# Kernel optimization log

Hardware: AMD Instinct MI355X
Metric: run time of the kernel (lower is better)

Reference implementation:

```python
import jax, jax.numpy as jnp
import numpy as np
import math

EPS = 1e-6
NUM_HEADS = 8


def _layernorm(x, g, b):
    mu = jnp.mean(x, axis=-1, keepdims=True)
    var = jnp.mean(jnp.square(x - mu), axis=-1, keepdims=True)
    return (x - mu) * jax.lax.rsqrt(var + EPS) * g + b


def _pos_embed(n, d):
    pos = jnp.arange(n, dtype=jnp.float32)[:, None]                  # [N,1]
    div = jnp.exp(jnp.arange(0, d, 2, dtype=jnp.float32) * (-math.log(10000.0) / d))
    ang = pos * div                                                  # [N,d/2]
    pe = jnp.stack([jnp.sin(ang), jnp.cos(ang)], axis=-1).reshape(n, d)
    return pe


def setup_inputs() -> dict:
    key = jax.random.key(0)
    B, N, C, L = 2, 2048, 256, 4
    ks = jax.random.split(key, 6)
    s = 0.02
    return {
        "x": jax.random.normal(ks[0], (B, N, C), jnp.float32),
        "qkv_w": jax.random.normal(ks[1], (L, C, 3 * C), jnp.float32) * s,
        "proj_w": jax.random.normal(ks[2], (L, C, C), jnp.float32) * s,
        "proj_b": jnp.zeros((L, C), jnp.float32),
        "w1": jax.random.normal(ks[3], (L, C, C), jnp.float32) * s,
        "b1": jnp.zeros((L, C), jnp.float32),
        "w2": jax.random.normal(ks[4], (L, C, C), jnp.float32) * s,
        "b2": jnp.zeros((L, C), jnp.float32),
        "g1": jnp.ones((L, C), jnp.float32),
        "be1": jnp.zeros((L, C), jnp.float32),
        "g2": jnp.ones((L, C), jnp.float32),
        "be2": jnp.zeros((L, C), jnp.float32),
    }


def reference(x, qkv_w, proj_w, proj_b, w1, b1, w2, b2, g1, be1, g2, be2):
    B, N, C = x.shape
    L = qkv_w.shape[0]
    H = NUM_HEADS
    dh = C // H
    scale = dh ** -0.5

    x = x + _pos_embed(N, C)[None]

    for l in range(L):
        # --- attention (manual QKV, post-norm residual as in source) ---
        qkv = (x @ qkv_w[l]).reshape(B, N, 3, H, dh)
        q, k, v = qkv[:, :, 0], qkv[:, :, 1], qkv[:, :, 2]           # [B,N,H,dh]
        attn = jnp.einsum('bqhd,bkhd->bhqk', q, k) * scale           # [B,H,N,N]
        attn = jax.nn.softmax(attn, axis=-1)
        o = jnp.einsum('bhqk,bkhd->bqhd', attn, v).reshape(B, N, C)
        o = o @ proj_w[l] + proj_b[l]
        x = _layernorm(x + o, g1[l], be1[l])
        # --- MLP (GELU exact, as torch nn.GELU default) ---
        m = jax.nn.gelu(x @ w1[l] + b1[l], approximate=False) @ w2[l] + b2[l]
        x = _layernorm(x + m, g2[l], be2[l])
    return x
```

## Files before the change

### kernel.cpp

```cpp
#include <hip/hip_runtime.h>
#include <math.h>

#define Bd 2
#define Nd 2048
#define Cd 256
#define Ld 4
#define Hd 8
#define Md (Bd*Nd)
#define BHd 16
#define U32d 1024
#define SPLITd 4

typedef __attribute__((ext_vector_type(8))) short bf16x8;
typedef __attribute__((ext_vector_type(4))) float f32x4;
typedef __attribute__((ext_vector_type(16))) float f32x16;
typedef __attribute__((ext_vector_type(4))) short shortx4;

static __device__ inline f32x4 mfma16(bf16x8 a, bf16x8 b, f32x4 c) {
    return __builtin_amdgcn_mfma_f32_16x16x32_bf16(a, b, c, 0, 0, 0);
}
static __device__ inline f32x16 mfma32(bf16x8 a, bf16x8 b, f32x16 c) {
    return __builtin_amdgcn_mfma_f32_32x32x16_bf16(a, b, c, 0, 0, 0);
}
static __device__ inline short f2bf(float f) {
    union { float f; unsigned u; } v; v.f = f;
    unsigned r = (v.u + 0x7fff + ((v.u >> 16) & 1)) >> 16;
    return (short)r;
}
static __device__ inline unsigned pkbf(float a, float b) {
    unsigned r;
    asm("v_cvt_pk_bf16_f32 %0, %1, %2" : "=v"(r) : "v"(a), "v"(b));
    return r;
}

__global__ __launch_bounds__(256)
void wtrans_kernel(const float* __restrict__ src, short* __restrict__ dst,
                   int Nc, float scale, int scaleLim)
{
    __shared__ float tile[32][33];
    int l = blockIdx.z;
    src += (size_t)l * 256 * Nc;
    dst += (size_t)l * Nc * 256;
    int c0 = blockIdx.x * 32, k0 = blockIdx.y * 32;
    int tx = threadIdx.x & 31, ty = threadIdx.x >> 5;
#pragma unroll
    for (int i = 0; i < 4; i++) {
        int k = ty + 8 * i;
        tile[k][tx] = src[(size_t)(k0 + k) * Nc + c0 + tx];
    }
    __syncthreads();
#pragma unroll
    for (int i = 0; i < 4; i++) {
        int cc = ty + 8 * i;
        int col = c0 + cc;
        float v = tile[tx][cc];
        if (col < scaleLim) v *= scale;
        dst[(size_t)col * 256 + k0 + tx] = f2bf(v);
    }
}

__global__ __launch_bounds__(256)
void pos_add_kernel(const float* __restrict__ xin, float* __restrict__ xf,
                    short* __restrict__ xb)
{
    int i = blockIdx.x * 256 + threadIdx.x;
    int c = i & (Cd - 1);
    int n = (i >> 8) & (Nd - 1);
    const float kneg = -9.210340371976184f / 256.0f;
    float div = __expf((float)(c & ~1) * kneg);
    float ang = (float)n * div;
    float pe = (c & 1) ? cosf(ang) : sinf(ang);
    float v = xin[i] + pe;
    xf[i] = v;
    xb[i] = f2bf(v);
}

__global__ __launch_bounds__(256)
void qkv_gemm_kernel(const short* __restrict__ Ab, const short* __restrict__ WT,
                     short* __restrict__ Qb, short* __restrict__ Kb,
                     short* __restrict__ Vtb)
{
    int t = threadIdx.x, w = t >> 6, l = t & 63, c = l & 15, g = l >> 4;
    int rowBase = blockIdx.y * 128 + w * 32;
    int colBase = blockIdx.x * 32;
    const f32x4 zero = {0.f, 0.f, 0.f, 0.f};
    f32x4 acc[2][2] = {{zero, zero}, {zero, zero}};
    const short* ap0 = Ab + (size_t)(rowBase + c) * 256 + g * 8;
    const short* ap1 = ap0 + 16 * 256;
    const short* bp0 = WT + (size_t)(colBase + c) * 256 + g * 8;
    const short* bp1 = bp0 + 16 * 256;
#pragma unroll
    for (int kc = 0; kc < 256; kc += 32) {
        bf16x8 a0 = *(const bf16x8*)(ap0 + kc);
        bf16x8 a1 = *(const bf16x8*)(ap1 + kc);
        bf16x8 b0 = *(const bf16x8*)(bp0 + kc);
        bf16x8 b1 = *(const bf16x8*)(bp1 + kc);
        acc[0][0] = mfma16(a0, b0, acc[0][0]);
        acc[0][1] = mfma16(a0, b1, acc[0][1]);
        acc[1][0] = mfma16(a1, b0, acc[1][0]);
        acc[1][1] = mfma16(a1, b1, acc[1][1]);
    }
    int region = colBase >> 8;
    if (region < 2) {
        short* dst = (region == 0) ? Qb : Kb;
        int cb = colBase - region * 256;
#pragma unroll
        for (int m = 0; m < 2; m++)
#pragma unroll
            for (int n = 0; n < 2; n++)
#pragma unroll
                for (int r = 0; r < 4; r++)
                    dst[(size_t)(rowBase + 16 * m + 4 * g + r) * 256 + cb + 16 * n + c]
                        = f2bf(acc[m][n][r]);
    } else {
        int b = rowBase >> 11;
        int ntok0 = (rowBase & (Nd - 1)) + 4 * g;
#pragma unroll
        for (int m = 0; m < 2; m++)
#pragma unroll
            for (int n = 0; n < 2; n++) {
                int chg = colBase - 512 + 16 * n + c;
                shortx4 pkv;
#pragma unroll
                for (int r = 0; r < 4; r++) pkv[r] = f2bf(acc[m][n][r]);
                *(shortx4*)&Vtb[(size_t)((b * Hd + (chg >> 5)) * 32 + (chg & 31)) * Nd
                                + ntok0 + 16 * m] = pkv;
            }
    }
}

__global__ __launch_bounds__(256)
void attn_part_kernel(const short* __restrict__ Qb, const short* __restrict__ Kb,
                      const short* __restrict__ Vtb, float* __restrict__ OP,
                      float* __restrict__ Lsum)
{
    int t = threadIdx.x, w = t >> 6, l = t & 63;
    int l5 = l >> 5, q32 = l & 31;
    bool low = (l5 == 0);
    int qt = blockIdx.x * 4 + w;
    int bh = blockIdx.y, part = blockIdx.z;
    int b = bh >> 3, h = bh & 7;

    bf16x8 qf0, qf1;
    {
        const short* qp = Qb + ((size_t)(b * Nd + qt * 32 + q32)) * 256 + h * 32 + 8 * l5;
        qf0 = *(const bf16x8*)qp;
        qf1 = *(const bf16x8*)(qp + 16);
    }
    const short* kp = Kb + (size_t)b * Nd * 256 + h * 32 + 8 * l5;
    const short* vp = Vtb + (size_t)(bh * 32 + q32) * Nd + 8 * l5;

    f32x16 O;
#pragma unroll
    for (int i = 0; i < 16; i++) O[i] = 0.f;
    float lsum = 0.f;

    const int kstart = part * (Nd / SPLITd);
    const int kend = (part + 1) * (Nd / SPLITd);

    bf16x8 kf[2][2], vv[4];
#pragma unroll
    for (int sb = 0; sb < 2; sb++)
#pragma unroll
        for (int ks = 0; ks < 2; ks++)
            kf[sb][ks] = *(const bf16x8*)(kp + (size_t)(kstart + 32 * sb + q32) * 256 + 16 * ks);
#pragma unroll
    for (int kc = 0; kc < 4; kc++)
        vv[kc] = *(const bf16x8*)(vp + kstart + 16 * kc);

    for (int k0 = kstart; k0 < kend; k0 += 64) {
        int kn = (k0 + 64 < kend) ? (k0 + 64) : k0;
        bf16x8 kfn[2][2], vvn[4];
#pragma unroll
        for (int sb = 0; sb < 2; sb++)
#pragma unroll
            for (int ks = 0; ks < 2; ks++)
                kfn[sb][ks] = *(const bf16x8*)(kp + (size_t)(kn + 32 * sb + q32) * 256 + 16 * ks);
#pragma unroll
        for (int kc = 0; kc < 4; kc++)
            vvn[kc] = *(const bf16x8*)(vp + kn + 16 * kc);

#pragma unroll
        for (int sb = 0; sb < 2; sb++) {
            f32x16 s;
#pragma unroll
            for (int i = 0; i < 16; i++) s[i] = 0.f;
            s = mfma32(kf[sb][0], qf0, s);
            s = mfma32(kf[sb][1], qf1, s);
            float ps = 0.f;
#pragma unroll
            for (int i = 0; i < 16; i++) { s[i] = exp2f(s[i]); ps += s[i]; }
            ps += __shfl_xor(ps, 32, 64);
            lsum += ps;
            unsigned wd[8];
#pragma unroll
            for (int i = 0; i < 8; i++) wd[i] = pkbf(s[2 * i], s[2 * i + 1]);
#pragma unroll
            for (int half = 0; half < 2; half++) {
                int b0 = 4 * half;
                unsigned sx0 = (unsigned)__shfl_xor((int)wd[b0], 32, 64);
                unsigned sx1 = (unsigned)__shfl_xor((int)wd[b0 + 1], 32, 64);
                unsigned sx2 = (unsigned)__shfl_xor((int)wd[b0 + 2], 32, 64);
                unsigned sx3 = (unsigned)__shfl_xor((int)wd[b0 + 3], 32, 64);
                union { unsigned u[4]; bf16x8 v; } pa;
                pa.u[0] = low ? wd[b0] : sx2;
                pa.u[1] = low ? wd[b0 + 1] : sx3;
                pa.u[2] = low ? sx0 : wd[b0 + 2];
                pa.u[3] = low ? sx1 : wd[b0 + 3];
                O = mfma32(pa.v, vv[2 * sb + half], O);
            }
        }
#pragma unroll
        for (int sb = 0; sb < 2; sb++)
#pragma unroll
            for (int ks = 0; ks < 2; ks++) kf[sb][ks] = kfn[sb][ks];
#pragma unroll
        for (int kc = 0; kc < 4; kc++) vv[kc] = vvn[kc];
    }

    int u = bh * 64 + qt;
    float* op = OP + ((size_t)part * U32d + u) * 1024;
#pragma unroll
    for (int i = 0; i < 16; i++) {
        int q = (i & 3) + 8 * (i >> 2) + 4 * l5;
        op[q * 32 + q32] = O[i];
    }
    if (low) Lsum[((size_t)part * U32d + u) * 32 + q32] = lsum;
}

__global__ __launch_bounds__(512)
void proj_ln_kernel(const float* __restrict__ OP, const float* __restrict__ Lsum,
                    const short* __restrict__ WT, const float* __restrict__ bias,
                    const float* __restrict__ resid, const float* __restrict__ gg,
                    const float* __restrict__ be, float* __restrict__ outf,
                    short* __restrict__ outb)
{
    __shared__ short Atile[16 * 264];
    __shared__ float red[8][16][2];
    int t = threadIdx.x;
    int rowBase = blockIdx.x * 16;

    {
        int r = t >> 5, seg = t & 31;
        int grow = rowBase + r;
        int bb = grow >> 11;
        int qt = (grow & (Nd - 1)) >> 5;
        int q = grow & 31;
        int h = seg >> 2;
        int dh0 = (seg & 3) * 8;
        int u = (bb * Hd + h) * 64 + qt;
        float o[8] = {0.f, 0.f, 0.f, 0.f, 0.f, 0.f, 0.f, 0.f};
        float L = 0.f;
#pragma unroll
        for (int p = 0; p < SPLITd; p++) {
            const float* src = OP + ((size_t)p * U32d + u) * 1024 + q * 32 + dh0;
            float4 v0 = *(const float4*)src;
            float4 v1 = *(const float4*)(src + 4);
            o[0] += v0.x; o[1] += v0.y; o[2] += v0.z; o[3] += v0.w;
            o[4] += v1.x; o[5] += v1.y; o[6] += v1.z; o[7] += v1.w;
            L += Lsum[((size_t)p * U32d + u) * 32 + q];
        }
        float inv = 1.f / L;
        bf16x8 pk;
#pragma unroll
        for (int j = 0; j < 8; j++) pk[j] = f2bf(o[j] * inv);
        *(bf16x8*)&Atile[r * 264 + seg * 8] = pk;
    }
    __syncthreads();

    int w = t >> 6, l = t & 63, c = l & 15, g = l >> 4;
    const f32x4 zero = {0.f, 0.f, 0.f, 0.f};
    f32x4 acc0 = zero, acc1 = zero;
    const short* bp0 = WT + (size_t)(w * 32 + c) * 256 + g * 8;
    const short* bp1 = bp0 + 16 * 256;
#pragma unroll
    for (int kc = 0; kc < 256; kc += 32) {
        bf16x8 a = *(const bf16x8*)&Atile[c * 264 + g * 8 + kc];
        acc0 = mfma16(a, *(const bf16x8*)(bp0 + kc), acc0);
        acc1 = mfma16(a, *(const bf16x8*)(bp1 + kc), acc1);
    }

    float vv[2][4], s_[4] = {0.f, 0.f, 0.f, 0.f}, sq_[4] = {0.f, 0.f, 0.f, 0.f};
    int col0 = w * 32 + c, col1 = col0 + 16;
    float bi0 = bias[col0], bi1 = bias[col1];
#pragma unroll
    for (int r = 0; r < 4; r++) {
        int row = rowBase + 4 * g + r;
        float v0 = acc0[r] + bi0 + resid[(size_t)row * 256 + col0];
        float v1 = acc1[r] + bi1 + resid[(size_t)row * 256 + col1];
        vv[0][r] = v0; vv[1][r] = v1;
        s_[r] += v0 + v1; sq_[r] += v0 * v0 + v1 * v1;
    }
#pragma unroll
    for (int off = 1; off <= 8; off <<= 1)
#pragma unroll
        for (int r = 0; r < 4; r++) {
            s_[r] += __shfl_xor(s_[r], off, 64);
            sq_[r] += __shfl_xor(sq_[r], off, 64);
        }
    if (c == 0)
#pragma unroll
        for (int r = 0; r < 4; r++) {
            red[w][4 * g + r][0] = s_[r];
            red[w][4 * g + r][1] = sq_[r];
        }
    __syncthreads();
    float mu[4], rs[4];
#pragma unroll
    for (int r = 0; r < 4; r++) {
        float S = 0.f, Q = 0.f;
#pragma unroll
        for (int ww = 0; ww < 8; ww++) { S += red[ww][4 * g + r][0]; Q += red[ww][4 * g + r][1]; }
        mu[r] = S * (1.f / 256.f);
        rs[r] = rsqrtf(Q * (1.f / 256.f) - mu[r] * mu[r] + 1e-6f);
    }
    float gv0 = gg[col0], bv0 = be[col0], gv1 = gg[col1], bv1 = be[col1];
#pragma unroll
    for (int r = 0; r < 4; r++) {
        int row = rowBase + 4 * g + r;
        float o0 = (vv[0][r] - mu[r]) * rs[r] * gv0 + bv0;
        float o1 = (vv[1][r] - mu[r]) * rs[r] * gv1 + bv1;
        outf[(size_t)row * 256 + col0] = o0;
        outf[(size_t)row * 256 + col1] = o1;
        outb[(size_t)row * 256 + col0] = f2bf(o0);
        outb[(size_t)row * 256 + col1] = f2bf(o1);
    }
}

template<int LAST>
__global__ __launch_bounds__(512)
void mlp_kernel(const short* __restrict__ xbin, const short* __restrict__ W1T,
                const float* __restrict__ b1, const short* __restrict__ W2T,
                const float* __restrict__ b2, const float* __restrict__ resid,
                const float* __restrict__ gg, const float* __restrict__ be,
                float* __restrict__ outf, short* __restrict__ outb)
{
    __shared__ short A1[16 * 264];
    __shared__ short A2[16 * 264];
    __shared__ float red[8][16][2];
    int t = threadIdx.x;
    int rowBase = blockIdx.x * 16;

    {
        int r = t >> 5, seg = t & 31;
        *(bf16x8*)&A1[r * 264 + seg * 8] =
            *(const bf16x8*)(xbin + (size_t)(rowBase + r) * 256 + seg * 8);
    }
    __syncthreads();

    int w = t >> 6, l = t & 63, c = l & 15, g = l >> 4;
    const f32x4 zero = {0.f, 0.f, 0.f, 0.f};
    int col0 = w * 32 + c, col1 = col0 + 16;

    {
        f32x4 acc0 = zero, acc1 = zero;
        const short* bp0 = W1T + (size_t)(w * 32 + c) * 256 + g * 8;
        const short* bp1 = bp0 + 16 * 256;
#pragma unroll
        for (int kc = 0; kc < 256; kc += 32) {
            bf16x8 a = *(const bf16x8*)&A1[c * 264 + g * 8 + kc];
            acc0 = mfma16(a, *(const bf16x8*)(bp0 + kc), acc0);
            acc1 = mfma16(a, *(const bf16x8*)(bp1 + kc), acc1);
        }
        float bi0 = b1[col0], bi1 = b1[col1];
#pragma unroll
        for (int r = 0; r < 4; r++) {
            float v0 = acc0[r] + bi0, v1 = acc1[r] + bi1;
            v0 = 0.5f * v0 * (1.f + erff(v0 * 0.7071067811865476f));
            v1 = 0.5f * v1 * (1.f + erff(v1 * 0.7071067811865476f));
            A2[(4 * g + r) * 264 + col0] = f2bf(v0);
            A2[(4 * g + r) * 264 + col1] = f2bf(v1);
        }
    }
    __syncthreads();

    f32x4 acc0 = zero, acc1 = zero;
    const short* bp0 = W2T + (size_t)(w * 32 + c) * 256 + g * 8;
    const short* bp1 = bp0 + 16 * 256;
#pragma unroll
    for (int kc = 0; kc < 256; kc += 32) {
        bf16x8 a = *(const bf16x8*)&A2[c * 264 + g * 8 + kc];
        acc0 = mfma16(a, *(const bf16x8*)(bp0 + kc), acc0);
        acc1 = mfma16(a, *(const bf16x8*)(bp1 + kc), acc1);
    }
    float vv[2][4], s_[4] = {0.f, 0.f, 0.f, 0.f}, sq_[4] = {0.f, 0.f, 0.f, 0.f};
    float bi0 = b2[col0], bi1 = b2[col1];
#pragma unroll
    for (int r = 0; r < 4; r++) {
        int row = rowBase + 4 * g + r;
        float v0 = acc0[r] + bi0 + resid[(size_t)row * 256 + col0];
        float v1 = acc1[r] + bi1 + resid[(size_t)row * 256 + col1];
        vv[0][r] = v0; vv[1][r] = v1;
        s_[r] += v0 + v1; sq_[r] += v0 * v0 + v1 * v1;
    }
#pragma unroll
    for (int off = 1; off <= 8; off <<= 1)
#pragma unroll
        for (int r = 0; r < 4; r++) {
            s_[r] += __shfl_xor(s_[r], off, 64);
            sq_[r] += __shfl_xor(sq_[r], off, 64);
        }
    if (c == 0)
#pragma unroll
        for (int r = 0; r < 4; r++) {
            red[w][4 * g + r][0] = s_[r];
            red[w][4 * g + r][1] = sq_[r];
        }
    __syncthreads();
    float mu[4], rs[4];
#pragma unroll
    for (int r = 0; r < 4; r++) {
        float S = 0.f, Q = 0.f;
#pragma unroll
        for (int ww = 0; ww < 8; ww++) { S += red[ww][4 * g + r][0]; Q += red[ww][4 * g + r][1]; }
        mu[r] = S * (1.f / 256.f);
        rs[r] = rsqrtf(Q * (1.f / 256.f) - mu[r] * mu[r] + 1e-6f);
    }
    float gv0 = gg[col0], bv0 = be[col0], gv1 = gg[col1], bv1 = be[col1];
#pragma unroll
    for (int r = 0; r < 4; r++) {
        int row = rowBase + 4 * g + r;
        float o0 = (vv[0][r] - mu[r]) * rs[r] * gv0 + bv0;
        float o1 = (vv[1][r] - mu[r]) * rs[r] * gv1 + bv1;
        outf[(size_t)row * 256 + col0] = o0;
        outf[(size_t)row * 256 + col1] = o1;
        if (!LAST) {
            outb[(size_t)row * 256 + col0] = f2bf(o0);
            outb[(size_t)row * 256 + col1] = f2bf(o1);
        }
    }
}

extern "C" void kernel_launch(void* const* d_in, const int* in_sizes, int n_in,
                              void* d_out, int out_size, void* d_ws, size_t ws_size,
                              hipStream_t stream)
{
    const float* x_in   = (const float*)d_in[0];
    const float* qkv_w  = (const float*)d_in[1];
    const float* proj_w = (const float*)d_in[2];
    const float* proj_b = (const float*)d_in[3];
    const float* w1     = (const float*)d_in[4];
    const float* b1     = (const float*)d_in[5];
    const float* w2     = (const float*)d_in[6];
    const float* b2     = (const float*)d_in[7];
    const float* g1     = (const float*)d_in[8];
    const float* be1    = (const float*)d_in[9];
    const float* g2     = (const float*)d_in[10];
    const float* be2    = (const float*)d_in[11];
    float* outp = (float*)d_out;

    char* p = (char*)d_ws;
    float* xf   = (float*)p;  p += (size_t)Md * Cd * 4;
    short* xb   = (short*)p;  p += (size_t)Md * Cd * 2;
    short* Qb   = (short*)p;  p += (size_t)Md * Cd * 2;
    short* Kb   = (short*)p;  p += (size_t)Md * Cd * 2;
    short* Vtb  = (short*)p;  p += (size_t)Md * Cd * 2;
    float* OP   = (float*)p;  p += (size_t)SPLITd * U32d * 1024 * 4;
    float* Lsum = (float*)p;  p += (size_t)SPLITd * U32d * 32 * 4;
    short* qkvT = (short*)p;  p += (size_t)Ld * 768 * 256 * 2;
    short* projT= (short*)p;  p += (size_t)Ld * 256 * 256 * 2;
    short* w1T  = (short*)p;  p += (size_t)Ld * 256 * 256 * 2;
    short* w2T  = (short*)p;  p += (size_t)Ld * 256 * 256 * 2;

    const float QSCALE = 0.17677669529663687f * 1.4426950408889634f;
    wtrans_kernel<<<dim3(24, 8, Ld), 256, 0, stream>>>(qkv_w, qkvT, 768, QSCALE, 256);
    wtrans_kernel<<<dim3(8, 8, Ld), 256, 0, stream>>>(proj_w, projT, 256, 1.f, 0);
    wtrans_kernel<<<dim3(8, 8, Ld), 256, 0, stream>>>(w1, w1T, 256, 1.f, 0);
    wtrans_kernel<<<dim3(8, 8, Ld), 256, 0, stream>>>(w2, w2T, 256, 1.f, 0);
    pos_add_kernel<<<Md * Cd / 256, 256, 0, stream>>>(x_in, xf, xb);

    for (int l = 0; l < Ld; l++) {
        qkv_gemm_kernel<<<dim3(24, 32), 256, 0, stream>>>(
            xb, qkvT + (size_t)l * 768 * 256, Qb, Kb, Vtb);
        attn_part_kernel<<<dim3(16, BHd, SPLITd), 256, 0, stream>>>(Qb, Kb, Vtb, OP, Lsum);
        proj_ln_kernel<<<Md / 16, 512, 0, stream>>>(
            OP, Lsum, projT + (size_t)l * 65536, proj_b + l * 256, xf,
            g1 + l * 256, be1 + l * 256, xf, xb);
        if (l == Ld - 1)
            mlp_kernel<1><<<Md / 16, 512, 0, stream>>>(
                xb, w1T + (size_t)l * 65536, b1 + l * 256,
                w2T + (size_t)l * 65536, b2 + l * 256, xf,
                g2 + l * 256, be2 + l * 256, outp, nullptr);
        else
            mlp_kernel<0><<<Md / 16, 512, 0, stream>>>(
                xb, w1T + (size_t)l * 65536, b1 + l * 256,
                w2T + (size_t)l * 65536, b2 + l * 256, xf,
                g2 + l * 256, be2 + l * 256, xf, xb);
    }
}
```

Baseline: 376.0 us.

## Fuse prep kernels, store attention partials as bf16, use permlane32 swap

Merges the four weight-transpose launches and the positional-add launch into one prep kernel to cut launch count. Attention partial outputs are packed to bf16 pairs instead of fp32, halving partial-output traffic between the attention and projection kernels at some precision cost. The cross-half shuffles in the softmax-to-PV repack are replaced with v_permlane32_swap, the row-sum shuffle moves out of the loop, and the redundant last-iteration prefetch is skipped.

Measured after the change: 374.5 us. About the same (-0.4%).

```diff
diff --git a/kernel.cpp b/kernel.cpp
--- a/kernel.cpp
+++ b/kernel.cpp
@@ -32,47 +32,57 @@
     asm("v_cvt_pk_bf16_f32 %0, %1, %2" : "=v"(r) : "v"(a), "v"(b));
     return r;
 }
+static __device__ inline float bf2f(unsigned u) {
+    return __uint_as_float((u & 0xffffu) << 16);
+}
 
 __global__ __launch_bounds__(256)
-void wtrans_kernel(const float* __restrict__ src, short* __restrict__ dst,
-                   int Nc, float scale, int scaleLim)
+void prep_kernel(const float* __restrict__ x_in, const float* __restrict__ qkv_w,
+                 const float* __restrict__ proj_w, const float* __restrict__ w1,
+                 const float* __restrict__ w2, float* __restrict__ xf,
+                 short* __restrict__ xb, short* __restrict__ qkvT,
+                 short* __restrict__ projT, short* __restrict__ w1T,
+                 short* __restrict__ w2T, float qscale)
 {
     __shared__ float tile[32][33];
-    int l = blockIdx.z;
-    src += (size_t)l * 256 * Nc;
-    dst += (size_t)l * Nc * 256;
-    int c0 = blockIdx.x * 32, k0 = blockIdx.y * 32;
-    int tx = threadIdx.x & 31, ty = threadIdx.x >> 5;
-#pragma unroll
-    for (int i = 0; i < 4; i++) {
-        int k = ty + 8 * i;
-        tile[k][tx] = src[(size_t)(k0 + k) * Nc + c0 + tx];
-    }
-    __syncthreads();
-#pragma unroll
-    for (int i = 0; i < 4; i++) {
-        int cc = ty + 8 * i;
-        int col = c0 + cc;
-        float v = tile[tx][cc];
-        if (col < scaleLim) v *= scale;
-        dst[(size_t)col * 256 + k0 + tx] = f2bf(v);
-    }
-}
-
-__global__ __launch_bounds__(256)
-void pos_add_kernel(const float* __restrict__ xin, float* __restrict__ xf,
-                    short* __restrict__ xb)
-{
-    int i = blockIdx.x * 256 + threadIdx.x;
-    int c = i & (Cd - 1);
-    int n = (i >> 8) & (Nd - 1);
-    const float kneg = -9.210340371976184f / 256.0f;
-    float div = __expf((float)(c & ~1) * kneg);
-    float ang = (float)n * div;
-    float pe = (c & 1) ? cosf(ang) : sinf(ang);
-    float v = xin[i] + pe;
-    xf[i] = v;
-    xb[i] = f2bf(v);
+    int id = blockIdx.x;
+    if (id < 1536) {
+        const float* src; short* dst; int Nc; float scale; int lim; int rem; int l;
+        if (id < 768)       { l = id / 192;         rem = id % 192; src = qkv_w;  dst = qkvT;  Nc = 768; scale = qscale; lim = 256; }
+        else if (id < 1024) { l = (id - 768) / 64;  rem = (id - 768) % 64;  src = proj_w; dst = projT; Nc = 256; scale = 1.f; lim = 0; }
+        else if (id < 1280) { l = (id - 1024) / 64; rem = (id - 1024) % 64; src = w1;     dst = w1T;   Nc = 256; scale = 1.f; lim = 0; }
+        else                { l = (id - 1280) / 64; rem = (id - 1280) % 64; src = w2;     dst = w2T;   Nc = 256; scale = 1.f; lim = 0; }
+        int nb = Nc >> 5;
+        int c0 = (rem % nb) * 32, k0 = (rem / nb) * 32;
+        src += (size_t)l * 256 * Nc;
+        dst += (size_t)l * Nc * 256;
+        int tx = threadIdx.x & 31, ty = threadIdx.x >> 5;
+#pragma unroll
+        for (int i = 0; i < 4; i++) {
+            int k = ty + 8 * i;
+            tile[k][tx] = src[(size_t)(k0 + k) * Nc + c0 + tx];
+        }
+        __syncthreads();
+#pragma unroll
+        for (int i = 0; i < 4; i++) {
+            int cc = ty + 8 * i;
+            int col = c0 + cc;
+            float v = tile[tx][cc];
+            if (col < lim) v *= scale;
+            dst[(size_t)col * 256 + k0 + tx] = f2bf(v);
+        }
+    } else {
+        int i = (id - 1536) * 256 + threadIdx.x;
+        int c = i & (Cd - 1);
+        int n = (i >> 8) & (Nd - 1);
+        const float kneg = -9.210340371976184f / 256.0f;
+        float div = __expf((float)(c & ~1) * kneg);
+        float ang = (float)n * div;
+        float pe = (c & 1) ? cosf(ang) : sinf(ang);
+        float v = x_in[i] + pe;
+        xf[i] = v;
+        xb[i] = f2bf(v);
+    }
 }
 
 __global__ __launch_bounds__(256)
@@ -131,12 +141,11 @@
 
 __global__ __launch_bounds__(256)
 void attn_part_kernel(const short* __restrict__ Qb, const short* __restrict__ Kb,
-                      const short* __restrict__ Vtb, float* __restrict__ OP,
+                      const short* __restrict__ Vtb, unsigned* __restrict__ OPb,
                       float* __restrict__ Lsum)
 {
     int t = threadIdx.x, w = t >> 6, l = t & 63;
     int l5 = l >> 5, q32 = l & 31;
-    bool low = (l5 == 0);
     int qt = blockIdx.x * 4 + w;
     int bh = blockIdx.y, part = blockIdx.z;
     int b = bh >> 3, h = bh & 7;
@@ -169,16 +178,19 @@
         vv[kc] = *(const bf16x8*)(vp + kstart + 16 * kc);
 
     for (int k0 = kstart; k0 < kend; k0 += 64) {
-        int kn = (k0 + 64 < kend) ? (k0 + 64) : k0;
+        bool has_next = (k0 + 64) < kend;
         bf16x8 kfn[2][2], vvn[4];
-#pragma unroll
-        for (int sb = 0; sb < 2; sb++)
-#pragma unroll
-            for (int ks = 0; ks < 2; ks++)
-                kfn[sb][ks] = *(const bf16x8*)(kp + (size_t)(kn + 32 * sb + q32) * 256 + 16 * ks);
-#pragma unroll
-        for (int kc = 0; kc < 4; kc++)
-            vvn[kc] = *(const bf16x8*)(vp + kn + 16 * kc);
+        if (has_next) {
+            int kn = k0 + 64;
+#pragma unroll
+            for (int sb = 0; sb < 2; sb++)
+#pragma unroll
+                for (int ks = 0; ks < 2; ks++)
+                    kfn[sb][ks] = *(const bf16x8*)(kp + (size_t)(kn + 32 * sb + q32) * 256 + 16 * ks);
+#pragma unroll
+            for (int kc = 0; kc < 4; kc++)
+                vvn[kc] = *(const bf16x8*)(vp + kn + 16 * kc);
+        }
 
 #pragma unroll
         for (int sb = 0; sb < 2; sb++) {
@@ -190,46 +202,45 @@
             float ps = 0.f;
 #pragma unroll
             for (int i = 0; i < 16; i++) { s[i] = exp2f(s[i]); ps += s[i]; }
-            ps += __shfl_xor(ps, 32, 64);
             lsum += ps;
             unsigned wd[8];
 #pragma unroll
             for (int i = 0; i < 8; i++) wd[i] = pkbf(s[2 * i], s[2 * i + 1]);
 #pragma unroll
             for (int half = 0; half < 2; half++) {
-                int b0 = 4 * half;
-                unsigned sx0 = (unsigned)__shfl_xor((int)wd[b0], 32, 64);
-                unsigned sx1 = (unsigned)__shfl_xor((int)wd[b0 + 1], 32, 64);
-                unsigned sx2 = (unsigned)__shfl_xor((int)wd[b0 + 2], 32, 64);
-                unsigned sx3 = (unsigned)__shfl_xor((int)wd[b0 + 3], 32, 64);
+                unsigned a0 = wd[4 * half], a1 = wd[4 * half + 1];
+                unsigned b0 = wd[4 * half + 2], b1 = wd[4 * half + 3];
+                asm("v_permlane32_swap_b32 %0, %1" : "+v"(a0), "+v"(b0));
+                asm("v_permlane32_swap_b32 %0, %1" : "+v"(a1), "+v"(b1));
                 union { unsigned u[4]; bf16x8 v; } pa;
-                pa.u[0] = low ? wd[b0] : sx2;
-                pa.u[1] = low ? wd[b0 + 1] : sx3;
-                pa.u[2] = low ? sx0 : wd[b0 + 2];
-                pa.u[3] = low ? sx1 : wd[b0 + 3];
+                pa.u[0] = a0; pa.u[1] = a1; pa.u[2] = b0; pa.u[3] = b1;
                 O = mfma32(pa.v, vv[2 * sb + half], O);
             }
         }
-#pragma unroll
-        for (int sb = 0; sb < 2; sb++)
-#pragma unroll
-            for (int ks = 0; ks < 2; ks++) kf[sb][ks] = kfn[sb][ks];
-#pragma unroll
-        for (int kc = 0; kc < 4; kc++) vv[kc] = vvn[kc];
-    }
+        if (has_next) {
+#pragma unroll
+            for (int sb = 0; sb < 2; sb++)
+#pragma unroll
+                for (int ks = 0; ks < 2; ks++) kf[sb][ks] = kfn[sb][ks];
+#pragma unroll
+            for (int kc = 0; kc < 4; kc++) vv[kc] = vvn[kc];
+        }
+    }
+
+    lsum += __shfl_xor(lsum, 32, 64);
 
     int u = bh * 64 + qt;
-    float* op = OP + ((size_t)part * U32d + u) * 1024;
-#pragma unroll
-    for (int i = 0; i < 16; i++) {
+    unsigned* opb = OPb + ((size_t)part * U32d + u) * 512;
+#pragma unroll
+    for (int i = 0; i < 16; i += 2) {
         int q = (i & 3) + 8 * (i >> 2) + 4 * l5;
-        op[q * 32 + q32] = O[i];
-    }
-    if (low) Lsum[((size_t)part * U32d + u) * 32 + q32] = lsum;
+        opb[(q >> 1) * 32 + q32] = pkbf(O[i], O[i + 1]);
+    }
+    if (l5 == 0) Lsum[((size_t)part * U32d + u) * 32 + q32] = lsum;
 }
 
 __global__ __launch_bounds__(512)
-void proj_ln_kernel(const float* __restrict__ OP, const float* __restrict__ Lsum,
+void proj_ln_kernel(const unsigned* __restrict__ OPb, const float* __restrict__ Lsum,
                     const short* __restrict__ WT, const float* __restrict__ bias,
                     const float* __restrict__ resid, const float* __restrict__ gg,
                     const float* __restrict__ be, float* __restrict__ outf,
@@ -249,15 +260,18 @@
         int h = seg >> 2;
         int dh0 = (seg & 3) * 8;
         int u = (bb * Hd + h) * 64 + qt;
+        int sh = (q & 1) * 16;
         float o[8] = {0.f, 0.f, 0.f, 0.f, 0.f, 0.f, 0.f, 0.f};
         float L = 0.f;
 #pragma unroll
         for (int p = 0; p < SPLITd; p++) {
-            const float* src = OP + ((size_t)p * U32d + u) * 1024 + q * 32 + dh0;
-            float4 v0 = *(const float4*)src;
-            float4 v1 = *(const float4*)(src + 4);
-            o[0] += v0.x; o[1] += v0.y; o[2] += v0.z; o[3] += v0.w;
-            o[4] += v1.x; o[5] += v1.y; o[6] += v1.z; o[7] += v1.w;
+            const unsigned* src = OPb + ((size_t)p * U32d + u) * 512 + (q >> 1) * 32 + dh0;
+            uint4 w0 = *(const uint4*)src;
+            uint4 w1 = *(const uint4*)(src + 4);
+            o[0] += bf2f(w0.x >> sh); o[1] += bf2f(w0.y >> sh);
+            o[2] += bf2f(w0.z >> sh); o[3] += bf2f(w0.w >> sh);
+            o[4] += bf2f(w1.x >> sh); o[5] += bf2f(w1.y >> sh);
+            o[6] += bf2f(w1.z >> sh); o[7] += bf2f(w1.w >> sh);
             L += Lsum[((size_t)p * U32d + u) * 32 + q];
         }
         float inv = 1.f / L;
@@ -450,31 +464,28 @@
     float* outp = (float*)d_out;
 
     char* p = (char*)d_ws;
-    float* xf   = (float*)p;  p += (size_t)Md * Cd * 4;
-    short* xb   = (short*)p;  p += (size_t)Md * Cd * 2;
-    short* Qb   = (short*)p;  p += (size_t)Md * Cd * 2;
-    short* Kb   = (short*)p;  p += (size_t)Md * Cd * 2;
-    short* Vtb  = (short*)p;  p += (size_t)Md * Cd * 2;
-    float* OP   = (float*)p;  p += (size_t)SPLITd * U32d * 1024 * 4;
-    float* Lsum = (float*)p;  p += (size_t)SPLITd * U32d * 32 * 4;
-    short* qkvT = (short*)p;  p += (size_t)Ld * 768 * 256 * 2;
-    short* projT= (short*)p;  p += (size_t)Ld * 256 * 256 * 2;
-    short* w1T  = (short*)p;  p += (size_t)Ld * 256 * 256 * 2;
-    short* w2T  = (short*)p;  p += (size_t)Ld * 256 * 256 * 2;
+    float* xf    = (float*)p;    p += (size_t)Md * Cd * 4;
+    short* xb    = (short*)p;    p += (size_t)Md * Cd * 2;
+    short* Qb    = (short*)p;    p += (size_t)Md * Cd * 2;
+    short* Kb    = (short*)p;    p += (size_t)Md * Cd * 2;
+    short* Vtb   = (short*)p;    p += (size_t)Md * Cd * 2;
+    unsigned* OPb = (unsigned*)p; p += (size_t)SPLITd * U32d * 512 * 4;
+    float* Lsum  = (float*)p;    p += (size_t)SPLITd * U32d * 32 * 4;
+    short* qkvT  = (short*)p;    p += (size_t)Ld * 768 * 256 * 2;
+    short* projT = (short*)p;    p += (size_t)Ld * 256 * 256 * 2;
+    short* w1T   = (short*)p;    p += (size_t)Ld * 256 * 256 * 2;
+    short* w2T   = (short*)p;    p += (size_t)Ld * 256 * 256 * 2;
 
     const float QSCALE = 0.17677669529663687f * 1.4426950408889634f;
-    wtrans_kernel<<<dim3(24, 8, Ld), 256, 0, stream>>>(qkv_w, qkvT, 768, QSCALE, 256);
-    wtrans_kernel<<<dim3(8, 8, Ld), 256, 0, stream>>>(proj_w, projT, 256, 1.f, 0);
-    wtrans_kernel<<<dim3(8, 8, Ld), 256, 0, stream>>>(w1, w1T, 256, 1.f, 0);
-    wtrans_kernel<<<dim3(8, 8, Ld), 256, 0, stream>>>(w2, w2T, 256, 1.f, 0);
-    pos_add_kernel<<<Md * Cd / 256, 256, 0, stream>>>(x_in, xf, xb);
+    prep_kernel<<<1536 + Md * Cd / 256, 256, 0, stream>>>(
+        x_in, qkv_w, proj_w, w1, w2, xf, xb, qkvT, projT, w1T, w2T, QSCALE);
 
     for (int l = 0; l < Ld; l++) {
         qkv_gemm_kernel<<<dim3(24, 32), 256, 0, stream>>>(
             xb, qkvT + (size_t)l * 768 * 256, Qb, Kb, Vtb);
-        attn_part_kernel<<<dim3(16, BHd, SPLITd), 256, 0, stream>>>(Qb, Kb, Vtb, OP, Lsum);
+        attn_part_kernel<<<dim3(16, BHd, SPLITd), 256, 0, stream>>>(Qb, Kb, Vtb, OPb, Lsum);
         proj_ln_kernel<<<Md / 16, 512, 0, stream>>>(
-            OP, Lsum, projT + (size_t)l * 65536, proj_b + l * 256, xf,
+            OPb, Lsum, projT + (size_t)l * 65536, proj_b + l * 256, xf,
             g1 + l * 256, be1 + l * 256, xf, xb);
         if (l == Ld - 1)
             mlp_kernel<1><<<Md / 16, 512, 0, stream>>>(
```
